# Kernel optimization log

Hardware: AMD Instinct MI355X
Metric: run time of the kernel (lower is better)

The kernel has to match this reference:

```python
import jax, jax.numpy as jnp
import numpy as np

DIM = 1024
DT_RANK = 64
D_STATE = 16
B, L = 4, 512


def _layer_norm(x, gamma, beta, eps=1e-6):
    mu = jnp.mean(x, axis=-1, keepdims=True)
    var = jnp.mean(jnp.square(x - mu), axis=-1, keepdims=True)
    return (x - mu) * jax.lax.rsqrt(var + eps) * gamma + beta


def _ssm(u, W_x, b_x, W_dt, b_dt, A_log, Dp):
    # u: [b, l, d]  (d = dim_inner)
    r = W_dt.shape[0]
    n = A_log.shape[1]
    A = -jnp.exp(A_log)                                   # [d, n]
    dbc = u @ W_x + b_x                                   # [b, l, r + 2n]
    delta = jax.nn.softplus(dbc[..., :r] @ W_dt + b_dt)   # [b, l, d]
    Bmat = dbc[..., r:r + n]                              # [b, l, n]
    Cmat = dbc[..., r + n:]                               # [b, l, n]
    dA = jnp.exp(jnp.einsum('bld,dn->bldn', delta, A))    # [b, l, d, n]
    dBu = jnp.einsum('bld,bln,bld->bldn', delta, Bmat, u) # [b, l, d, n]

    def step(h, xs):
        dA_t, dBu_t, C_t = xs
        h = dA_t * h + dBu_t                              # [b, d, n]
        y = jnp.einsum('bdn,bn->bd', h, C_t)
        return h, y

    h0 = jnp.zeros((u.shape[0], u.shape[2], n), u.dtype)
    _, ys = jax.lax.scan(
        step, h0,
        (jnp.swapaxes(dA, 0, 1), jnp.swapaxes(dBu, 0, 1), jnp.swapaxes(Cmat, 0, 1)))
    y = jnp.swapaxes(ys, 0, 1)                            # [b, l, d]
    return y + u * Dp


def setup_inputs() -> dict:
    key = jax.random.key(0)
    ks = jax.random.split(key, 16)
    s = 0.02
    d, r, n = DIM, DT_RANK, D_STATE
    inp = {
        'inputs': jax.random.normal(ks[0], (B, L, d), jnp.float32),
        'gamma': jnp.ones((d,), jnp.float32),
        'beta': jnp.zeros((d,), jnp.float32),
        'W_proj': jax.random.normal(ks[1], (d, d), jnp.float32) * s,
        'b_proj': jnp.zeros((d,), jnp.float32),
        'W_fc': jax.random.normal(ks[2], (d, d), jnp.float32) * s,
        'b_fc': jnp.zeros((d,), jnp.float32),
        'W_bc': jax.random.normal(ks[3], (d, d), jnp.float32) * s,
        'b_bc': jnp.zeros((d,), jnp.float32),
        'W_x1': jax.random.normal(ks[4], (d, r + 2 * n), jnp.float32) * s,
        'b_x1': jnp.zeros((r + 2 * n,), jnp.float32),
        'W_dt1': jax.random.normal(ks[5], (r, d), jnp.float32) * s,
        'b_dt1': jnp.full((d,), -4.0, jnp.float32),
        'A_log1': jnp.log(jnp.broadcast_to(jnp.arange(1, n + 1, dtype=jnp.float32), (d, n))),
        'D1': jnp.ones((d,), jnp.float32),
        'W_x2': jax.random.normal(ks[6], (d, r + 2 * n), jnp.float32) * s,
        'b_x2': jnp.zeros((r + 2 * n,), jnp.float32),
        'W_dt2': jax.random.normal(ks[7], (r, d), jnp.float32) * s,
        'b_dt2': jnp.full((d,), -4.0, jnp.float32),
        'A_log2': jnp.log(jnp.broadcast_to(jnp.arange(1, n + 1, dtype=jnp.float32), (d, n))),
        'D2': jnp.ones((d,), jnp.float32),
    }
    return inp


def reference(inputs, gamma, beta, W_proj, b_proj, W_fc, b_fc, W_bc, b_bc,
              W_x1, b_x1, W_dt1, b_dt1, A_log1, D1,
              W_x2, b_x2, W_dt2, b_dt2, A_log2, D2):
    skip = inputs
    x = _layer_norm(inputs, gamma, beta)
    proj = x @ W_proj + b_proj           # same Dense called twice in original
    z = jax.nn.silu(proj)
    # forward direction: 1x1 conv (== dense) -> softplus -> SSM
    u1 = jax.nn.softplus(proj @ W_fc + b_fc)
    y1 = _ssm(u1, W_x1, b_x1, W_dt1, b_dt1, A_log1, D1)
    # backward direction branch (original does not flip the sequence)
    u2 = jax.nn.softplus(proj @ W_bc + b_bc)
    y2 = _ssm(u2, W_x2, b_x2, W_dt2, b_dt2, A_log2, D2)
    return y1 * z + y2 * z + skip
```

## Files before the change

### kernel.cpp

```cpp
#include <hip/hip_runtime.h>
#include <hip/hip_bf16.h>
#include <math.h>

#define DIM 1024
#define NTOK 2048
#define LSEQ 512
#define NB 4
#define DTR 64
#define DST 16
#define NCH 8
#define TCH 64

typedef unsigned short ushort_t;
typedef __attribute__((ext_vector_type(8))) short bf16x8;
typedef __attribute__((ext_vector_type(4))) float f32x4;

__device__ __forceinline__ float softplus_f(float x) {
    return (x > 20.f) ? x : log1pf(__expf(x));
}
__device__ __forceinline__ ushort_t to_bf16_bits(float f) {
    __hip_bfloat16 h = __float2bfloat16(f);
    return *(ushort_t*)&h;
}
__device__ __forceinline__ float bf16_bits_to_f(ushort_t b) {
    return __uint_as_float(((unsigned int)b) << 16);
}
template<int CTRL>
__device__ __forceinline__ float dpp_add(float x) {
    int xi = __float_as_int(x);
    int yi = __builtin_amdgcn_update_dpp(xi, xi, CTRL, 0xF, 0xF, false);
    return x + __int_as_float(yi);
}

__global__ __launch_bounds__(256) void wconv_kernel(
    const float* __restrict__ W0, const float* __restrict__ W1, const float* __restrict__ W2,
    ushort_t* __restrict__ T0, ushort_t* __restrict__ T1, ushort_t* __restrict__ T2) {
    const float* W = blockIdx.z == 0 ? W0 : blockIdx.z == 1 ? W1 : W2;
    ushort_t* T    = blockIdx.z == 0 ? T0 : blockIdx.z == 1 ? T1 : T2;
    __shared__ float tile[64][65];
    const int k0 = blockIdx.x * 64, n0 = blockIdx.y * 64;
    const int tid = threadIdx.x;
    #pragma unroll
    for (int p = 0; p < 16; ++p) {
        int idx = p * 256 + tid;
        int i = idx >> 6, j = idx & 63;
        tile[i][j] = W[(size_t)(k0 + i) * DIM + n0 + j];
    }
    __syncthreads();
    #pragma unroll
    for (int p = 0; p < 16; ++p) {
        int idx = p * 256 + tid;
        int j = idx >> 6, i = idx & 63;
        T[(size_t)(n0 + j) * DIM + k0 + i] = to_bf16_bits(tile[i][j]);
    }
}

__global__ __launch_bounds__(256) void ln_kernel(
    const float* __restrict__ x, const float* __restrict__ gamma,
    const float* __restrict__ beta, ushort_t* __restrict__ out) {
    const int row = blockIdx.x;
    const int tid = threadIdx.x;
    const float4* xr = (const float4*)(x + (size_t)row * DIM);
    float4 v = xr[tid];
    float s  = v.x + v.y + v.z + v.w;
    float sq = v.x*v.x + v.y*v.y + v.z*v.z + v.w*v.w;
    for (int o = 32; o > 0; o >>= 1) {
        s  += __shfl_down(s, o);
        sq += __shfl_down(sq, o);
    }
    __shared__ float red[8];
    if ((tid & 63) == 0) { red[tid >> 6] = s; red[4 + (tid >> 6)] = sq; }
    __syncthreads();
    float st  = red[0] + red[1] + red[2] + red[3];
    float sqt = red[4] + red[5] + red[6] + red[7];
    float mu = st * (1.f / DIM);
    float var = sqt * (1.f / DIM) - mu * mu;
    float rstd = rsqrtf(var + 1e-6f);
    float4 g = ((const float4*)gamma)[tid];
    float4 bt = ((const float4*)beta)[tid];
    ushort4 ob;
    ob.x = to_bf16_bits((v.x - mu) * rstd * g.x + bt.x);
    ob.y = to_bf16_bits((v.y - mu) * rstd * g.y + bt.y);
    ob.z = to_bf16_bits((v.z - mu) * rstd * g.z + bt.z);
    ob.w = to_bf16_bits((v.w - mu) * rstd * g.w + bt.w);
    ((ushort4*)(out + (size_t)row * DIM))[tid] = ob;
}

template<int ACT>
__global__ __launch_bounds__(256) void mfma_gemm(
    const ushort_t* __restrict__ A, const ushort_t* __restrict__ Bt,
    const float* __restrict__ bias, ushort_t* __restrict__ outb, float* __restrict__ outf) {
    __shared__ __align__(16) ushort_t Asl[2][64 * 64];
    __shared__ __align__(16) ushort_t Bsl[2][64 * 64];
    const int tid = threadIdx.x;
    const int bm = blockIdx.y * 64;
    const int bn = blockIdx.x * 64;
    const int lane = tid & 63;
    const int wid = tid >> 6;
    const int r  = lane & 15;
    const int kg = lane >> 4;
    const int wm = wid >> 1, wn = wid & 1;

    f32x4 acc[2][2] = {};

    auto STAGE = [&](int buf, int k0) {
        #pragma unroll
        for (int q = 0; q < 2; ++q) {
            int c = q * 256 + tid;
            int row = c >> 3;
            int ksl = ((c & 7) ^ (row & 7)) << 3;
            __builtin_amdgcn_global_load_lds(
                (const __attribute__((address_space(1))) void*)(A + (size_t)(bm + row) * DIM + k0 + ksl),
                (__attribute__((address_space(3))) void*)(&Asl[buf][c * 8]), 16, 0, 0);
        }
        #pragma unroll
        for (int q = 0; q < 2; ++q) {
            int c = q * 256 + tid;
            int row = c >> 3;
            int ksl = ((c & 7) ^ (row & 7)) << 3;
            __builtin_amdgcn_global_load_lds(
                (const __attribute__((address_space(1))) void*)(Bt + (size_t)(bn + row) * DIM + k0 + ksl),
                (__attribute__((address_space(3))) void*)(&Bsl[buf][c * 8]), 16, 0, 0);
        }
    };

    STAGE(0, 0);
    __syncthreads();
    int cur = 0;
    for (int t = 0; t < DIM / 64; ++t) {
        if (t + 1 < DIM / 64) STAGE(cur ^ 1, (t + 1) * 64);
        #pragma unroll
        for (int kk = 0; kk < 2; ++kk) {
            const int sw = ((kk * 4 + kg) ^ (r & 7)) << 3;
            bf16x8 af[2], bfr[2];
            #pragma unroll
            for (int mi = 0; mi < 2; ++mi)
                af[mi] = *(const bf16x8*)&Asl[cur][(wm * 32 + mi * 16 + r) * 64 + sw];
            #pragma unroll
            for (int nj = 0; nj < 2; ++nj)
                bfr[nj] = *(const bf16x8*)&Bsl[cur][(wn * 32 + nj * 16 + r) * 64 + sw];
            #pragma unroll
            for (int mi = 0; mi < 2; ++mi)
                #pragma unroll
                for (int nj = 0; nj < 2; ++nj)
                    acc[mi][nj] = __builtin_amdgcn_mfma_f32_16x16x32_bf16(af[mi], bfr[nj], acc[mi][nj], 0, 0, 0);
        }
        __syncthreads();
        cur ^= 1;
    }

    #pragma unroll
    for (int nj = 0; nj < 2; ++nj) {
        const int col = bn + wn * 32 + nj * 16 + r;
        const float bv = bias[col];
        #pragma unroll
        for (int mi = 0; mi < 2; ++mi) {
            const int rowb = bm + wm * 32 + mi * 16 + kg * 4;
            #pragma unroll
            for (int j = 0; j < 4; ++j) {
                float v = acc[mi][nj][j] + bv;
                size_t idx = (size_t)(rowb + j) * DIM + col;
                if (ACT == 0) {
                    outb[idx] = to_bf16_bits(v);
                    outf[idx] = v / (1.f + __expf(-v));
                } else if (ACT == 1) {
                    float sp = softplus_f(v);
                    outf[idx] = sp;
                    outb[idx] = to_bf16_bits(sp);
                } else {
                    outb[idx] = to_bf16_bits(softplus_f(v));
                }
            }
        }
    }
}

__global__ __launch_bounds__(256) void wcomb_kernel(
    const float* __restrict__ Wx1, const float* __restrict__ Wdt1,
    const float* __restrict__ bx1, const float* __restrict__ bdt1,
    const float* __restrict__ Wx2, const float* __restrict__ Wdt2,
    const float* __restrict__ bx2, const float* __restrict__ bdt2,
    ushort_t* __restrict__ WcombT, ushort_t* __restrict__ WxBCt,
    float* __restrict__ bcomb) {
    const int s = blockIdx.z;
    const float* __restrict__ Wx  = s ? Wx2  : Wx1;
    const float* __restrict__ Wdt = s ? Wdt2 : Wdt1;
    const float* __restrict__ bx  = s ? bx2  : bx1;
    const float* __restrict__ bdt = s ? bdt2 : bdt1;
    const int tid = threadIdx.x;
    __shared__ float Xs[64][65];
    __shared__ float Ds[64][65];
    if (blockIdx.y == 16) {
        const int i0 = blockIdx.x * 64;
        #pragma unroll
        for (int p = 0; p < 8; ++p) {
            int idx = p * 256 + tid;
            int c = idx >> 6, i = i0 + (idx & 63);
            WxBCt[((size_t)s * 32 + c) * DIM + i] = to_bf16_bits(Wx[(size_t)i * 96 + 64 + c]);
        }
        if (tid < 64) {
            int j = i0 + tid;
            float acc = bdt[j];
            for (int r = 0; r < 64; ++r) acc = fmaf(bx[r], Wdt[(size_t)r * DIM + j], acc);
            bcomb[(size_t)s * DIM + j] = acc;
        }
        return;
    }
    const int i0 = blockIdx.x * 64, j0 = blockIdx.y * 64;
    #pragma unroll
    for (int p = 0; p < 16; ++p) {
        int idx = p * 256 + tid;
        int i = idx >> 6, r = idx & 63;
        Xs[i][r] = Wx[(size_t)(i0 + i) * 96 + r];
    }
    #pragma unroll
    for (int p = 0; p < 16; ++p) {
        int idx = p * 256 + tid;
        int r = idx >> 6, j = idx & 63;
        Ds[r][j] = Wdt[(size_t)r * DIM + j0 + j];
    }
    __syncthreads();
    const int tj = (tid >> 4) * 4, ti = (tid & 15) * 4;
    float acc[4][4] = {};
    for (int r = 0; r < 64; ++r) {
        float a[4], b[4];
        #pragma unroll
        for (int q = 0; q < 4; ++q) a[q] = Ds[r][tj + q];
        #pragma unroll
        for (int q = 0; q < 4; ++q) b[q] = Xs[ti + q][r];
        #pragma unroll
        for (int ji = 0; ji < 4; ++ji)
            #pragma unroll
            for (int ii = 0; ii < 4; ++ii)
                acc[ji][ii] = fmaf(a[ji], b[ii], acc[ji][ii]);
    }
    #pragma unroll
    for (int ji = 0; ji < 4; ++ji)
        #pragma unroll
        for (int ii = 0; ii < 4; ++ii)
            WcombT[((size_t)s * DIM + j0 + tj + ji) * DIM + i0 + ti + ii] = to_bf16_bits(acc[ji][ii]);
}

__global__ __launch_bounds__(256) void bc_kernel(
    const ushort_t* __restrict__ u1b, const ushort_t* __restrict__ u2b,
    const ushort_t* __restrict__ WxBCt,
    const float* __restrict__ bx1, const float* __restrict__ bx2,
    float* __restrict__ BC) {
    const int s = blockIdx.z;
    const ushort_t* __restrict__ u  = s ? u2b : u1b;
    const ushort_t* __restrict__ Bt = WxBCt + (size_t)s * 32 * DIM;
    const float* __restrict__ bx    = s ? bx2 : bx1;
    const int bm = blockIdx.x * 64;
    const int kbase = blockIdx.y * 256;
    __shared__ __align__(16) ushort_t Asl[2][64 * 64];
    __shared__ __align__(16) ushort_t Bsl[2][32 * 64];
    const int tid = threadIdx.x;
    const int lane = tid & 63, wid = tid >> 6;
    const int r = lane & 15, kg = lane >> 4;
    f32x4 acc[2] = {};
    auto STAGE = [&](int buf, int k0) {
        #pragma unroll
        for (int q = 0; q < 2; ++q) {
            int c = q * 256 + tid;
            int row = c >> 3;
            int ksl = ((c & 7) ^ (row & 7)) << 3;
            __builtin_amdgcn_global_load_lds(
                (const __attribute__((address_space(1))) void*)(u + (size_t)(bm + row) * DIM + k0 + ksl),
                (__attribute__((address_space(3))) void*)(&Asl[buf][c * 8]), 16, 0, 0);
        }
        {
            int c = tid;
            int row = c >> 3;
            int ksl = ((c & 7) ^ (row & 7)) << 3;
            __builtin_amdgcn_global_load_lds(
                (const __attribute__((address_space(1))) void*)(Bt + (size_t)row * DIM + k0 + ksl),
                (__attribute__((address_space(3))) void*)(&Bsl[buf][c * 8]), 16, 0, 0);
        }
    };
    STAGE(0, kbase);
    __syncthreads();
    int cur = 0;
    for (int t = 0; t < 4; ++t) {
        if (t + 1 < 4) STAGE(cur ^ 1, kbase + (t + 1) * 64);
        #pragma unroll
        for (int kk = 0; kk < 2; ++kk) {
            const int sw = ((kk * 4 + kg) ^ (r & 7)) << 3;
            bf16x8 af = *(const bf16x8*)&Asl[cur][(wid * 16 + r) * 64 + sw];
            #pragma unroll
            for (int nj = 0; nj < 2; ++nj) {
                bf16x8 bfr = *(const bf16x8*)&Bsl[cur][(nj * 16 + r) * 64 + sw];
                acc[nj] = __builtin_amdgcn_mfma_f32_16x16x32_bf16(af, bfr, acc[nj], 0, 0, 0);
            }
        }
        __syncthreads();
        cur ^= 1;
    }
    const bool kc0 = (blockIdx.y == 0);
    #pragma unroll
    for (int nj = 0; nj < 2; ++nj) {
        const int col = nj * 16 + r;
        #pragma unroll
        for (int j = 0; j < 4; ++j) {
            const int row = bm + wid * 16 + kg * 4 + j;
            float v = acc[nj][j];
            if (kc0) v += bx[64 + col];
            atomicAdd(&BC[((size_t)s * NTOK + row) * 32 + col], v);
        }
    }
}

#define CH 4
#define SLOAD1(S, base) do { \
    _Pragma("unroll") for (int j_ = 0; j_ < CH; ++j_) { \
        const size_t rr_ = rowbase + (base) + j_; \
        dl##S[j_] = bf16_bits_to_f(delta[rr_ * DIM + d]); \
        uu##S[j_] = u[rr_ * DIM + d]; \
        Bn##S[j_] = BCp[rr_ * 32 + n]; \
    } \
} while (0)
#define SCOMP1(S) do { \
    _Pragma("unroll") for (int j_ = 0; j_ < CH; ++j_) { \
        float e_ = __expf(dl##S[j_] * a); \
        h = fmaf(e_, h, dl##S[j_] * Bn##S[j_] * uu##S[j_]); \
        sd += dl##S[j_]; \
    } \
} while (0)

__global__ __launch_bounds__(256) void scan_pass1(
    const ushort_t* __restrict__ delta1, const float* __restrict__ u1c,
    const float* __restrict__ Alog1,
    const ushort_t* __restrict__ delta2, const float* __restrict__ u2c,
    const float* __restrict__ Alog2, const float* __restrict__ BC,
    float* __restrict__ rbuf, float* __restrict__ sdbuf) {
    const int s = blockIdx.z;
    const ushort_t* __restrict__ delta = s ? delta2 : delta1;
    const float* __restrict__ u    = s ? u2c   : u1c;
    const float* __restrict__ Alog = s ? Alog2 : Alog1;
    const float* __restrict__ BCp  = BC + (size_t)s * NTOK * 32;
    const int tid = threadIdx.x;
    const int n = tid & 15;
    const int d = blockIdx.x * 16 + (tid >> 4);
    const int b = blockIdx.y >> 3;
    const int c = blockIdx.y & 7;
    const float a = -__expf(Alog[d * DST + n]);
    const size_t rowbase = (size_t)b * LSEQ + (size_t)c * TCH;
    float h = 0.f, sd = 0.f;
    float dlA[CH], uuA[CH], BnA[CH];
    float dlB[CH], uuB[CH], BnB[CH];
    SLOAD1(A, 0);
    for (int t = 0; t < TCH; t += 2 * CH) {
        SLOAD1(B, t + CH);
        SCOMP1(A);
        if (t + 2 * CH < TCH) SLOAD1(A, t + 2 * CH);
        SCOMP1(B);
    }
    const size_t ridx = ((((size_t)s * NB + b) * NCH + c) * DIM + d) * DST + n;
    rbuf[ridx] = h;
    if (n == 0) sdbuf[(((size_t)s * NB + b) * NCH + c) * DIM + d] = sd;
}

__global__ __launch_bounds__(256) void scan_combine(
    const float* __restrict__ Alog1, const float* __restrict__ Alog2,
    float* __restrict__ rbuf, const float* __restrict__ sdbuf) {
    const int tid = threadIdx.x;
    const int sb = blockIdx.x >> 6;
    const int s = sb >> 2, b = sb & 3;
    const int flat = (blockIdx.x & 63) * 256 + tid;
    const int d = flat >> 4, n = flat & 15;
    const float* Alog = s ? Alog2 : Alog1;
    const float a = -__expf(Alog[d * DST + n]);
    float hprev = 0.f;
    #pragma unroll
    for (int c = 0; c < NCH; ++c) {
        const size_t ridx = ((((size_t)s * NB + b) * NCH + c) * DIM + d) * DST + n;
        float rc = rbuf[ridx];
        float P = __expf(a * sdbuf[(((size_t)s * NB + b) * NCH + c) * DIM + d]);
        float hnew = fmaf(P, hprev, rc);
        rbuf[ridx] = hprev;
        hprev = hnew;
    }
}

#define SLOAD2(S, base) do { \
    _Pragma("unroll") for (int j_ = 0; j_ < CH; ++j_) { \
        const size_t rr_ = rowbase + (base) + j_; \
        dl##S[j_] = bf16_bits_to_f(delta[rr_ * DIM + d]); \
        uu##S[j_] = u[rr_ * DIM + d]; \
        Bn##S[j_] = BCp[rr_ * 32 + n]; \
        Cn##S[j_] = BCp[rr_ * 32 + 16 + n]; \
    } \
} while (0)
#define SCOMP2(S, base) do { \
    _Pragma("unroll") for (int j_ = 0; j_ < CH; ++j_) { \
        float e_ = __expf(dl##S[j_] * a); \
        h = fmaf(e_, h, dl##S[j_] * Bn##S[j_] * uu##S[j_]); \
        float p_ = h * Cn##S[j_]; \
        p_ = dpp_add<0xB1>(p_); \
        p_ = dpp_add<0x4E>(p_); \
        p_ = dpp_add<0x124>(p_); \
        p_ = dpp_add<0x128>(p_); \
        if (n == 0) y[(rowbase + (base) + j_) * DIM + d] = fmaf(uu##S[j_], dcf, p_); \
    } \
} while (0)

__global__ __launch_bounds__(256) void scan_pass2(
    const ushort_t* __restrict__ delta1, const float* __restrict__ u1c,
    const float* __restrict__ Alog1, const float* __restrict__ D1p, float* __restrict__ y1,
    const ushort_t* __restrict__ delta2, const float* __restrict__ u2c,
    const float* __restrict__ Alog2, const float* __restrict__ D2p, float* __restrict__ y2,
    const float* __restrict__ BC, const float* __restrict__ rbuf) {
    const int s = blockIdx.z;
    const ushort_t* __restrict__ delta = s ? delta2 : delta1;
    const float* __restrict__ u    = s ? u2c   : u1c;
    const float* __restrict__ Alog = s ? Alog2 : Alog1;
    const float* __restrict__ Dp   = s ? D2p   : D1p;
    float* __restrict__ y          = s ? y2    : y1;
    const float* __restrict__ BCp  = BC + (size_t)s * NTOK * 32;
    const int tid = threadIdx.x;
    const int n = tid & 15;
    const int d = blockIdx.x * 16 + (tid >> 4);
    const int b = blockIdx.y >> 3;
    const int c = blockIdx.y & 7;
    const float a = -__expf(Alog[d * DST + n]);
    const float dcf = Dp[d];
    const size_t rowbase = (size_t)b * LSEQ + (size_t)c * TCH;
    float h = rbuf[((((size_t)s * NB + b) * NCH + c) * DIM + d) * DST + n];
    float dlA[CH], uuA[CH], BnA[CH], CnA[CH];
    float dlB[CH], uuB[CH], BnB[CH], CnB[CH];
    SLOAD2(A, 0);
    for (int t = 0; t < TCH; t += 2 * CH) {
        SLOAD2(B, t + CH);
        SCOMP2(A, t);
        if (t + 2 * CH < TCH) SLOAD2(A, t + 2 * CH);
        SCOMP2(B, t + CH);
    }
}

__global__ __launch_bounds__(256) void final_kernel(
    const float* __restrict__ y1, const float* __restrict__ y2,
    const float* __restrict__ skip, float* io) {
    const int i = blockIdx.x * 256 + threadIdx.x;
    float4 a = ((const float4*)y1)[i];
    float4 b = ((const float4*)y2)[i];
    float4 sk = ((const float4*)skip)[i];
    float4 z = ((float4*)io)[i];
    float4 o;
    o.x = (a.x + b.x) * z.x + sk.x;
    o.y = (a.y + b.y) * z.y + sk.y;
    o.z = (a.z + b.z) * z.z + sk.z;
    o.w = (a.w + b.w) * z.w + sk.w;
    ((float4*)io)[i] = o;
}

extern "C" void kernel_launch(void* const* d_in, const int* in_sizes, int n_in,
                              void* d_out, int out_size, void* d_ws, size_t ws_size,
                              hipStream_t stream) {
    const float* inputs = (const float*)d_in[0];
    const float* gamma  = (const float*)d_in[1];
    const float* beta   = (const float*)d_in[2];
    const float* W_proj = (const float*)d_in[3];
    const float* b_proj = (const float*)d_in[4];
    const float* W_fc   = (const float*)d_in[5];
    const float* b_fc   = (const float*)d_in[6];
    const float* W_bc   = (const float*)d_in[7];
    const float* b_bc   = (const float*)d_in[8];
    const float* W_x1   = (const float*)d_in[9];
    const float* b_x1   = (const float*)d_in[10];
    const float* W_dt1  = (const float*)d_in[11];
    const float* b_dt1  = (const float*)d_in[12];
    const float* A_log1 = (const float*)d_in[13];
    const float* D1     = (const float*)d_in[14];
    const float* W_x2   = (const float*)d_in[15];
    const float* b_x2   = (const float*)d_in[16];
    const float* W_dt2  = (const float*)d_in[17];
    const float* b_dt2  = (const float*)d_in[18];
    const float* A_log2 = (const float*)d_in[19];
    const float* D2     = (const float*)d_in[20];
    float* out = (float*)d_out;
    char* wsb  = (char*)d_ws;

    ushort_t* xln_bf  = (ushort_t*)wsb;
    ushort_t* proj_bf = (ushort_t*)(wsb + (4u << 20));
    float*    y1      = (float*)wsb;
    float*    u1      = (float*)(wsb + (8u << 20));
    float*    u2      = (float*)(wsb + (16u << 20));
    ushort_t* u1b     = (ushort_t*)(wsb + (24u << 20));
    ushort_t* u2b     = (ushort_t*)(wsb + (28u << 20));
    float*    y2      = (float*)(wsb + (24u << 20));
    ushort_t* delta1  = (ushort_t*)(wsb + (32u << 20));
    ushort_t* delta2  = (ushort_t*)(wsb + (36u << 20));
    ushort_t* WtP     = (ushort_t*)(wsb + (40u << 20));
    ushort_t* WtF     = (ushort_t*)(wsb + (42u << 20));
    ushort_t* WtB     = (ushort_t*)(wsb + (44u << 20));
    ushort_t* WxBCt   = (ushort_t*)(wsb + (40u << 20));
    float*    bcomb   = (float*)(wsb + (41u << 20));
    ushort_t* WcombT  = (ushort_t*)(wsb + (42u << 20));
    float*    rbuf    = (float*)(wsb + (42u << 20));
    float*    BC      = (float*)(wsb + (46u << 20));
    float*    sdbuf   = (float*)(wsb + (46u << 20) + (512u << 10));
    float*    zbuf    = out;

    wconv_kernel<<<dim3(16, 16, 3), 256, 0, stream>>>(W_proj, W_fc, W_bc, WtP, WtF, WtB);
    ln_kernel<<<NTOK, 256, 0, stream>>>(inputs, gamma, beta, xln_bf);
    mfma_gemm<0><<<dim3(DIM / 64, NTOK / 64), 256, 0, stream>>>(xln_bf, WtP, b_proj, proj_bf, zbuf);
    mfma_gemm<1><<<dim3(DIM / 64, NTOK / 64), 256, 0, stream>>>(proj_bf, WtF, b_fc, u1b, u1);
    mfma_gemm<1><<<dim3(DIM / 64, NTOK / 64), 256, 0, stream>>>(proj_bf, WtB, b_bc, u2b, u2);
    wcomb_kernel<<<dim3(16, 17, 2), 256, 0, stream>>>(W_x1, W_dt1, b_x1, b_dt1,
                                                      W_x2, W_dt2, b_x2, b_dt2,
                                                      WcombT, WxBCt, bcomb);
    hipMemsetAsync(BC, 0, (size_t)2 * NTOK * 32 * sizeof(float), stream);
    bc_kernel<<<dim3(NTOK / 64, 4, 2), 256, 0, stream>>>(u1b, u2b, WxBCt, b_x1, b_x2, BC);
    mfma_gemm<2><<<dim3(DIM / 64, NTOK / 64), 256, 0, stream>>>(u1b, WcombT, bcomb, delta1, nullptr);
    mfma_gemm<2><<<dim3(DIM / 64, NTOK / 64), 256, 0, stream>>>(u2b, WcombT + (size_t)DIM * DIM,
                                                                bcomb + DIM, delta2, nullptr);
    scan_pass1<<<dim3(DIM / 16, NB * NCH, 2), 256, 0, stream>>>(delta1, u1, A_log1,
                                                                delta2, u2, A_log2, BC, rbuf, sdbuf);
    scan_combine<<<512, 256, 0, stream>>>(A_log1, A_log2, rbuf, sdbuf);
    scan_pass2<<<dim3(DIM / 16, NB * NCH, 2), 256, 0, stream>>>(delta1, u1, A_log1, D1, y1,
                                                                delta2, u2, A_log2, D2, y2, BC, rbuf);
    final_kernel<<<(size_t)NTOK * DIM / 4 / 256, 256, 0, stream>>>(y1, y2, inputs, out);
}
```

Baseline: 313.7 us.

## Fuse chunked scan passes into one kernel with transposed delta/u/BC layouts

The GEMM epilogues now write delta and u in bf16, transposed to a [dim][token] layout. The B/C projection accumulates into a transposed BC buffer. The three scan kernels (pass1, combine, pass2) become a single kernel in which each block handles two channels for one batch. The block runs the chunk prefix in shared memory, so the rbuf/sdbuf global round trips and two launches go away, and each thread can do contiguous vector loads along time. In exchange, u in the scan drops from fp32 to bf16, the transposed epilogue stores are strided, and the grid has fewer threads per channel-chunk.

```diff
diff --git a/kernel.cpp b/kernel.cpp
--- a/kernel.cpp
+++ b/kernel.cpp
@@ -89,7 +89,8 @@
 template<int ACT>
 __global__ __launch_bounds__(256) void mfma_gemm(
     const ushort_t* __restrict__ A, const ushort_t* __restrict__ Bt,
-    const float* __restrict__ bias, ushort_t* __restrict__ outb, float* __restrict__ outf) {
+    const float* __restrict__ bias, ushort_t* __restrict__ outb,
+    ushort_t* __restrict__ outbT, float* __restrict__ outf) {
     __shared__ __align__(16) ushort_t Asl[2][64 * 64];
     __shared__ __align__(16) ushort_t Bsl[2][64 * 64];
     const int tid = threadIdx.x;
@@ -156,20 +157,28 @@
         #pragma unroll
         for (int mi = 0; mi < 2; ++mi) {
             const int rowb = bm + wm * 32 + mi * 16 + kg * 4;
-            #pragma unroll
-            for (int j = 0; j < 4; ++j) {
-                float v = acc[mi][nj][j] + bv;
-                size_t idx = (size_t)(rowb + j) * DIM + col;
-                if (ACT == 0) {
+            if (ACT == 0) {
+                #pragma unroll
+                for (int j = 0; j < 4; ++j) {
+                    float v = acc[mi][nj][j] + bv;
+                    size_t idx = (size_t)(rowb + j) * DIM + col;
                     outb[idx] = to_bf16_bits(v);
                     outf[idx] = v / (1.f + __expf(-v));
-                } else if (ACT == 1) {
-                    float sp = softplus_f(v);
-                    outf[idx] = sp;
-                    outb[idx] = to_bf16_bits(sp);
-                } else {
-                    outb[idx] = to_bf16_bits(softplus_f(v));
                 }
+            } else {
+                float sp[4];
+                #pragma unroll
+                for (int j = 0; j < 4; ++j)
+                    sp[j] = softplus_f(acc[mi][nj][j] + bv);
+                if (ACT == 1) {
+                    #pragma unroll
+                    for (int j = 0; j < 4; ++j)
+                        outb[(size_t)(rowb + j) * DIM + col] = to_bf16_bits(sp[j]);
+                }
+                ushort4 tp;
+                tp.x = to_bf16_bits(sp[0]); tp.y = to_bf16_bits(sp[1]);
+                tp.z = to_bf16_bits(sp[2]); tp.w = to_bf16_bits(sp[3]);
+                *(ushort4*)&outbT[(size_t)col * NTOK + rowb] = tp;
             }
         }
     }
@@ -245,7 +254,7 @@
     const ushort_t* __restrict__ u1b, const ushort_t* __restrict__ u2b,
     const ushort_t* __restrict__ WxBCt,
     const float* __restrict__ bx1, const float* __restrict__ bx2,
-    float* __restrict__ BC) {
+    float* __restrict__ BCT) {
     const int s = blockIdx.z;
     const ushort_t* __restrict__ u  = s ? u2b : u1b;
     const ushort_t* __restrict__ Bt = WxBCt + (size_t)s * 32 * DIM;
@@ -304,135 +313,98 @@
             const int row = bm + wid * 16 + kg * 4 + j;
             float v = acc[nj][j];
             if (kc0) v += bx[64 + col];
-            atomicAdd(&BC[((size_t)s * NTOK + row) * 32 + col], v);
-        }
-    }
-}
-
-#define CH 4
-#define SLOAD1(S, base) do { \
-    _Pragma("unroll") for (int j_ = 0; j_ < CH; ++j_) { \
-        const size_t rr_ = rowbase + (base) + j_; \
-        dl##S[j_] = bf16_bits_to_f(delta[rr_ * DIM + d]); \
-        uu##S[j_] = u[rr_ * DIM + d]; \
-        Bn##S[j_] = BCp[rr_ * 32 + n]; \
-    } \
-} while (0)
-#define SCOMP1(S) do { \
-    _Pragma("unroll") for (int j_ = 0; j_ < CH; ++j_) { \
-        float e_ = __expf(dl##S[j_] * a); \
-        h = fmaf(e_, h, dl##S[j_] * Bn##S[j_] * uu##S[j_]); \
-        sd += dl##S[j_]; \
-    } \
-} while (0)
-
-__global__ __launch_bounds__(256) void scan_pass1(
-    const ushort_t* __restrict__ delta1, const float* __restrict__ u1c,
-    const float* __restrict__ Alog1,
-    const ushort_t* __restrict__ delta2, const float* __restrict__ u2c,
-    const float* __restrict__ Alog2, const float* __restrict__ BC,
-    float* __restrict__ rbuf, float* __restrict__ sdbuf) {
+            atomicAdd(&BCT[((size_t)s * 32 + col) * NTOK + row], v);
+        }
+    }
+}
+
+__global__ __launch_bounds__(256) void scan_fused(
+    const ushort_t* __restrict__ dT1, const ushort_t* __restrict__ uT1,
+    const float* __restrict__ Alog1, const float* __restrict__ D1p, float* __restrict__ y1,
+    const ushort_t* __restrict__ dT2, const ushort_t* __restrict__ uT2,
+    const float* __restrict__ Alog2, const float* __restrict__ D2p, float* __restrict__ y2,
+    const float* __restrict__ BCT) {
     const int s = blockIdx.z;
-    const ushort_t* __restrict__ delta = s ? delta2 : delta1;
-    const float* __restrict__ u    = s ? u2c   : u1c;
-    const float* __restrict__ Alog = s ? Alog2 : Alog1;
-    const float* __restrict__ BCp  = BC + (size_t)s * NTOK * 32;
-    const int tid = threadIdx.x;
-    const int n = tid & 15;
-    const int d = blockIdx.x * 16 + (tid >> 4);
-    const int b = blockIdx.y >> 3;
-    const int c = blockIdx.y & 7;
+    const ushort_t* __restrict__ dT = s ? dT2 : dT1;
+    const ushort_t* __restrict__ uT = s ? uT2 : uT1;
+    const float* __restrict__ Alog  = s ? Alog2 : Alog1;
+    const float* __restrict__ Dp    = s ? D2p : D1p;
+    float* __restrict__ y           = s ? y2 : y1;
+    const int tid = threadIdx.x;
+    const int n  = tid & 15;
+    const int c  = (tid >> 4) & 7;
+    const int dd = tid >> 7;
+    const int d  = blockIdx.x * 2 + dd;
+    const int b  = blockIdx.y;
+    const int tok0 = b * LSEQ + c * TCH;
     const float a = -__expf(Alog[d * DST + n]);
-    const size_t rowbase = (size_t)b * LSEQ + (size_t)c * TCH;
+
+    const ushort_t* __restrict__ dlp = dT + d * NTOK + tok0;
+    const ushort_t* __restrict__ uup = uT + d * NTOK + tok0;
+    const float* __restrict__ Bp = BCT + (s * 32 + n) * NTOK + tok0;
+    const float* __restrict__ Cp = Bp + 16 * NTOK;
+
+    __shared__ float rL[2][16][8];
+    __shared__ float sdL[2][8];
+    __shared__ float hinL[2][16][8];
+
     float h = 0.f, sd = 0.f;
-    float dlA[CH], uuA[CH], BnA[CH];
-    float dlB[CH], uuB[CH], BnB[CH];
-    SLOAD1(A, 0);
-    for (int t = 0; t < TCH; t += 2 * CH) {
-        SLOAD1(B, t + CH);
-        SCOMP1(A);
-        if (t + 2 * CH < TCH) SLOAD1(A, t + 2 * CH);
-        SCOMP1(B);
-    }
-    const size_t ridx = ((((size_t)s * NB + b) * NCH + c) * DIM + d) * DST + n;
-    rbuf[ridx] = h;
-    if (n == 0) sdbuf[(((size_t)s * NB + b) * NCH + c) * DIM + d] = sd;
-}
-
-__global__ __launch_bounds__(256) void scan_combine(
-    const float* __restrict__ Alog1, const float* __restrict__ Alog2,
-    float* __restrict__ rbuf, const float* __restrict__ sdbuf) {
-    const int tid = threadIdx.x;
-    const int sb = blockIdx.x >> 6;
-    const int s = sb >> 2, b = sb & 3;
-    const int flat = (blockIdx.x & 63) * 256 + tid;
-    const int d = flat >> 4, n = flat & 15;
-    const float* Alog = s ? Alog2 : Alog1;
-    const float a = -__expf(Alog[d * DST + n]);
-    float hprev = 0.f;
-    #pragma unroll
-    for (int c = 0; c < NCH; ++c) {
-        const size_t ridx = ((((size_t)s * NB + b) * NCH + c) * DIM + d) * DST + n;
-        float rc = rbuf[ridx];
-        float P = __expf(a * sdbuf[(((size_t)s * NB + b) * NCH + c) * DIM + d]);
-        float hnew = fmaf(P, hprev, rc);
-        rbuf[ridx] = hprev;
-        hprev = hnew;
-    }
-}
-
-#define SLOAD2(S, base) do { \
-    _Pragma("unroll") for (int j_ = 0; j_ < CH; ++j_) { \
-        const size_t rr_ = rowbase + (base) + j_; \
-        dl##S[j_] = bf16_bits_to_f(delta[rr_ * DIM + d]); \
-        uu##S[j_] = u[rr_ * DIM + d]; \
-        Bn##S[j_] = BCp[rr_ * 32 + n]; \
-        Cn##S[j_] = BCp[rr_ * 32 + 16 + n]; \
-    } \
-} while (0)
-#define SCOMP2(S, base) do { \
-    _Pragma("unroll") for (int j_ = 0; j_ < CH; ++j_) { \
-        float e_ = __expf(dl##S[j_] * a); \
-        h = fmaf(e_, h, dl##S[j_] * Bn##S[j_] * uu##S[j_]); \
-        float p_ = h * Cn##S[j_]; \
-        p_ = dpp_add<0xB1>(p_); \
-        p_ = dpp_add<0x4E>(p_); \
-        p_ = dpp_add<0x124>(p_); \
-        p_ = dpp_add<0x128>(p_); \
-        if (n == 0) y[(rowbase + (base) + j_) * DIM + d] = fmaf(uu##S[j_], dcf, p_); \
-    } \
-} while (0)
-
-__global__ __launch_bounds__(256) void scan_pass2(
-    const ushort_t* __restrict__ delta1, const float* __restrict__ u1c,
-    const float* __restrict__ Alog1, const float* __restrict__ D1p, float* __restrict__ y1,
-    const ushort_t* __restrict__ delta2, const float* __restrict__ u2c,
-    const float* __restrict__ Alog2, const float* __restrict__ D2p, float* __restrict__ y2,
-    const float* __restrict__ BC, const float* __restrict__ rbuf) {
-    const int s = blockIdx.z;
-    const ushort_t* __restrict__ delta = s ? delta2 : delta1;
-    const float* __restrict__ u    = s ? u2c   : u1c;
-    const float* __restrict__ Alog = s ? Alog2 : Alog1;
-    const float* __restrict__ Dp   = s ? D2p   : D1p;
-    float* __restrict__ y          = s ? y2    : y1;
-    const float* __restrict__ BCp  = BC + (size_t)s * NTOK * 32;
-    const int tid = threadIdx.x;
-    const int n = tid & 15;
-    const int d = blockIdx.x * 16 + (tid >> 4);
-    const int b = blockIdx.y >> 3;
-    const int c = blockIdx.y & 7;
-    const float a = -__expf(Alog[d * DST + n]);
+    for (int t = 0; t < TCH; t += 8) {
+        bf16x8 dl8 = *(const bf16x8*)(dlp + t);
+        bf16x8 uu8 = *(const bf16x8*)(uup + t);
+        f32x4 B0 = *(const f32x4*)(Bp + t);
+        f32x4 B1 = *(const f32x4*)(Bp + t + 4);
+        #pragma unroll
+        for (int j = 0; j < 8; ++j) {
+            float dl = bf16_bits_to_f((ushort_t)dl8[j]);
+            float uu = bf16_bits_to_f((ushort_t)uu8[j]);
+            float Bn = (j < 4) ? B0[j] : B1[j - 4];
+            float e  = __expf(dl * a);
+            h = fmaf(e, h, dl * Bn * uu);
+            sd += dl;
+        }
+    }
+    rL[dd][n][c] = h;
+    if (n == 0) sdL[dd][c] = sd;
+    __syncthreads();
+    if (tid < 32) {
+        const int dc = tid >> 4, nc = tid & 15;
+        const float ac = -__expf(Alog[(blockIdx.x * 2 + dc) * DST + nc]);
+        float hp = 0.f;
+        #pragma unroll
+        for (int cc = 0; cc < 8; ++cc) {
+            float P  = __expf(ac * sdL[dc][cc]);
+            float rc = rL[dc][nc][cc];
+            hinL[dc][nc][cc] = hp;
+            hp = fmaf(P, hp, rc);
+        }
+    }
+    __syncthreads();
+    h = hinL[dd][n][c];
     const float dcf = Dp[d];
-    const size_t rowbase = (size_t)b * LSEQ + (size_t)c * TCH;
-    float h = rbuf[((((size_t)s * NB + b) * NCH + c) * DIM + d) * DST + n];
-    float dlA[CH], uuA[CH], BnA[CH], CnA[CH];
-    float dlB[CH], uuB[CH], BnB[CH], CnB[CH];
-    SLOAD2(A, 0);
-    for (int t = 0; t < TCH; t += 2 * CH) {
-        SLOAD2(B, t + CH);
-        SCOMP2(A, t);
-        if (t + 2 * CH < TCH) SLOAD2(A, t + 2 * CH);
-        SCOMP2(B, t + CH);
+    float* __restrict__ yp = y + (size_t)tok0 * DIM + d;
+    for (int t = 0; t < TCH; t += 8) {
+        bf16x8 dl8 = *(const bf16x8*)(dlp + t);
+        bf16x8 uu8 = *(const bf16x8*)(uup + t);
+        f32x4 B0 = *(const f32x4*)(Bp + t);
+        f32x4 B1 = *(const f32x4*)(Bp + t + 4);
+        f32x4 C0 = *(const f32x4*)(Cp + t);
+        f32x4 C1 = *(const f32x4*)(Cp + t + 4);
+        #pragma unroll
+        for (int j = 0; j < 8; ++j) {
+            float dl = bf16_bits_to_f((ushort_t)dl8[j]);
+            float uu = bf16_bits_to_f((ushort_t)uu8[j]);
+            float Bn = (j < 4) ? B0[j] : B1[j - 4];
+            float Cn = (j < 4) ? C0[j] : C1[j - 4];
+            float e  = __expf(dl * a);
+            h = fmaf(e, h, dl * Bn * uu);
+            float p = h * Cn;
+            p = dpp_add<0xB1>(p);
+            p = dpp_add<0x4E>(p);
+            p = dpp_add<0x124>(p);
+            p = dpp_add<0x128>(p);
+            if (n == 0) yp[(t + j) * DIM] = fmaf(uu, dcf, p);
+        }
     }
 }
 
@@ -479,44 +451,39 @@
     float* out = (float*)d_out;
     char* wsb  = (char*)d_ws;
 
-    ushort_t* xln_bf  = (ushort_t*)wsb;
-    ushort_t* proj_bf = (ushort_t*)(wsb + (4u << 20));
-    float*    y1      = (float*)wsb;
-    float*    u1      = (float*)(wsb + (8u << 20));
-    float*    u2      = (float*)(wsb + (16u << 20));
-    ushort_t* u1b     = (ushort_t*)(wsb + (24u << 20));
-    ushort_t* u2b     = (ushort_t*)(wsb + (28u << 20));
-    float*    y2      = (float*)(wsb + (24u << 20));
-    ushort_t* delta1  = (ushort_t*)(wsb + (32u << 20));
-    ushort_t* delta2  = (ushort_t*)(wsb + (36u << 20));
-    ushort_t* WtP     = (ushort_t*)(wsb + (40u << 20));
-    ushort_t* WtF     = (ushort_t*)(wsb + (42u << 20));
-    ushort_t* WtB     = (ushort_t*)(wsb + (44u << 20));
-    ushort_t* WxBCt   = (ushort_t*)(wsb + (40u << 20));
-    float*    bcomb   = (float*)(wsb + (41u << 20));
-    ushort_t* WcombT  = (ushort_t*)(wsb + (42u << 20));
-    float*    rbuf    = (float*)(wsb + (42u << 20));
-    float*    BC      = (float*)(wsb + (46u << 20));
-    float*    sdbuf   = (float*)(wsb + (46u << 20) + (512u << 10));
-    float*    zbuf    = out;
+    ushort_t* xln_bf   = (ushort_t*)wsb;
+    ushort_t* proj_bf  = (ushort_t*)(wsb + (4u << 20));
+    float*    y1       = (float*)wsb;
+    ushort_t* u1t      = (ushort_t*)(wsb + (8u << 20));
+    ushort_t* u2t      = (ushort_t*)(wsb + (12u << 20));
+    float*    y2       = (float*)(wsb + (16u << 20));
+    ushort_t* u1b      = (ushort_t*)(wsb + (24u << 20));
+    ushort_t* u2b      = (ushort_t*)(wsb + (28u << 20));
+    ushort_t* delta1T  = (ushort_t*)(wsb + (32u << 20));
+    ushort_t* delta2T  = (ushort_t*)(wsb + (36u << 20));
+    ushort_t* WtP      = (ushort_t*)(wsb + (40u << 20));
+    ushort_t* WtF      = (ushort_t*)(wsb + (42u << 20));
+    ushort_t* WtB      = (ushort_t*)(wsb + (44u << 20));
+    ushort_t* WxBCt    = (ushort_t*)(wsb + (40u << 20));
+    float*    bcomb    = (float*)(wsb + (41u << 20));
+    ushort_t* WcombT   = (ushort_t*)(wsb + (42u << 20));
+    float*    BCT      = (float*)(wsb + (46u << 20));
+    float*    zbuf     = out;
 
     wconv_kernel<<<dim3(16, 16, 3), 256, 0, stream>>>(W_proj, W_fc, W_bc, WtP, WtF, WtB);
     ln_kernel<<<NTOK, 256, 0, stream>>>(inputs, gamma, beta, xln_bf);
-    mfma_gemm<0><<<dim3(DIM / 64, NTOK / 64), 256, 0, stream>>>(xln_bf, WtP, b_proj, proj_bf, zbuf);
-    mfma_gemm<1><<<dim3(DIM / 64, NTOK / 64), 256, 0, stream>>>(proj_bf, WtF, b_fc, u1b, u1);
-    mfma_gemm<1><<<dim3(DIM / 64, NTOK / 64), 256, 0, stream>>>(proj_bf, WtB, b_bc, u2b, u2);
+    mfma_gemm<0><<<dim3(DIM / 64, NTOK / 64), 256, 0, stream>>>(xln_bf, WtP, b_proj, proj_bf, nullptr, zbuf);
+    mfma_gemm<1><<<dim3(DIM / 64, NTOK / 64), 256, 0, stream>>>(proj_bf, WtF, b_fc, u1b, u1t, nullptr);
+    mfma_gemm<1><<<dim3(DIM / 64, NTOK / 64), 256, 0, stream>>>(proj_bf, WtB, b_bc, u2b, u2t, nullptr);
     wcomb_kernel<<<dim3(16, 17, 2), 256, 0, stream>>>(W_x1, W_dt1, b_x1, b_dt1,
                                                       W_x2, W_dt2, b_x2, b_dt2,
                                                       WcombT, WxBCt, bcomb);
-    hipMemsetAsync(BC, 0, (size_t)2 * NTOK * 32 * sizeof(float), stream);
-    bc_kernel<<<dim3(NTOK / 64, 4, 2), 256, 0, stream>>>(u1b, u2b, WxBCt, b_x1, b_x2, BC);
-    mfma_gemm<2><<<dim3(DIM / 64, NTOK / 64), 256, 0, stream>>>(u1b, WcombT, bcomb, delta1, nullptr);
+    hipMemsetAsync(BCT, 0, (size_t)2 * 32 * NTOK * sizeof(float), stream);
+    bc_kernel<<<dim3(NTOK / 64, 4, 2), 256, 0, stream>>>(u1b, u2b, WxBCt, b_x1, b_x2, BCT);
+    mfma_gemm<2><<<dim3(DIM / 64, NTOK / 64), 256, 0, stream>>>(u1b, WcombT, bcomb, nullptr, delta1T, nullptr);
     mfma_gemm<2><<<dim3(DIM / 64, NTOK / 64), 256, 0, stream>>>(u2b, WcombT + (size_t)DIM * DIM,
-                                                                bcomb + DIM, delta2, nullptr);
-    scan_pass1<<<dim3(DIM / 16, NB * NCH, 2), 256, 0, stream>>>(delta1, u1, A_log1,
-                                                                delta2, u2, A_log2, BC, rbuf, sdbuf);
-    scan_combine<<<512, 256, 0, stream>>>(A_log1, A_log2, rbuf, sdbuf);
-    scan_pass2<<<dim3(DIM / 16, NB * NCH, 2), 256, 0, stream>>>(delta1, u1, A_log1, D1, y1,
-                                                                delta2, u2, A_log2, D2, y2, BC, rbuf);
+                                                                bcomb + DIM, nullptr, delta2T, nullptr);
+    scan_fused<<<dim3(DIM / 2, NB, 2), 256, 0, stream>>>(delta1T, u1t, A_log1, D1, y1,
+                                                         delta2T, u2t, A_log2, D2, y2, BCT);
     final_kernel<<<(size_t)NTOK * DIM / 4 / 256, 256, 0, stream>>>(y1, y2, inputs, out);
 }
```

Measured after the change: 403.2 us. 1.29x slower.
